# Kernel optimization log

Hardware: AMD Instinct MI355X
Metric: run time of the kernel (lower is better)

Reference implementation:

```python
import jax, jax.numpy as jnp
import numpy as np

B, S = 64, 200
DK = 32           # d_k = d_a = d_e
NQ = 4096         # n_question
NE = 20000        # n_exercise
NAT = 2000
NIT = 2000


def _xavier(k, shape):
    a = float(np.sqrt(6.0 / (shape[0] + shape[1])))
    return jax.random.uniform(k, shape, jnp.float32, -a, a)


def setup_inputs() -> dict:
    key = jax.random.key(0)
    ks = jax.random.split(key, 24)
    d = {}
    d['e_data'] = jax.random.randint(ks[0], (B, S), 0, NE)
    d['at_data'] = jax.random.randint(ks[1], (B, S), 0, NAT)
    d['it_data'] = jax.random.randint(ks[2], (B, S), 0, NIT)
    d['a_data'] = jax.random.randint(ks[3], (B, S), 0, 2).astype(jnp.float32)
    # binary Q-matrix: ~64 skills per exercise on average
    d['q_matrix'] = (jax.random.uniform(ks[4], (NE + 10, NQ + 1)) < (64.0 / NQ)).astype(jnp.float32)
    d['E_e'] = _xavier(ks[5], (NE + 10, DK))
    d['E_at'] = _xavier(ks[6], (NAT + 10, DK))
    d['E_it'] = _xavier(ks[7], (NIT + 10, DK))
    d['W1'] = _xavier(ks[8], (DK, 3 * DK)); d['b1'] = jnp.zeros((DK,), jnp.float32)
    d['W2'] = _xavier(ks[9], (DK, 4 * DK)); d['b2'] = jnp.zeros((DK,), jnp.float32)
    d['W3'] = _xavier(ks[10], (DK, 4 * DK)); d['b3'] = jnp.zeros((DK,), jnp.float32)
    d['W4'] = _xavier(ks[11], (DK, 3 * DK)); d['b4'] = jnp.zeros((DK,), jnp.float32)
    d['W5'] = _xavier(ks[12], (DK, 2 * DK)); d['b5'] = jnp.zeros((DK,), jnp.float32)
    d['h0'] = _xavier(ks[13], (NQ + 1, DK))
    return d


def _forward(e_data, at_data, it_data, a_data, q_matrix, E_e, E_at, E_it,
             W1, b1, W2, b2, W3, b3, W4, b4, W5, b5, h0):
    e_emb = E_e[e_data]                    # [B,S,DK]
    at_emb = E_at[at_data]                 # [B,S,DK]
    it_emb = E_it[it_data]                 # [B,S,DK]
    a_rep = jnp.broadcast_to(a_data[:, :, None], (B, S, DK))  # repeat answer to d_a
    all_learning = jnp.einsum('bsf,kf->bsk', jnp.concatenate([e_emb, at_emb, a_rep], -1), W1) + b1

    h_pre0 = jnp.broadcast_to(h0[None], (B, NQ + 1, DK))
    h_tilde0 = jnp.einsum('bn,bnd->bd', q_matrix[e_data[:, 0]], h_pre0)
    W4h, W4l, W4i = W4[:, :DK], W4[:, DK:2 * DK], W4[:, 2 * DK:]

    def step(carry, xs):
        learning_pre, h_pre, h_tilde_pre = carry
        e_t, it, learning, e_next_emb, e_next = xs
        q_e = q_matrix[e_t]                               # [B,NQ+1] gather
        x = jnp.concatenate([learning_pre, it, learning, h_tilde_pre], -1)  # [B,4DK]
        lg = jnp.tanh(x @ W2.T + b2)
        gl = jax.nn.sigmoid(x @ W3.T + b3)
        LG = gl * (lg + 1.0) * 0.5                        # [B,DK]
        LG_tilde = q_e[:, :, None] * LG[:, None, :]       # scatter (outer product), dropout off (eval)
        gamma_f = jax.nn.sigmoid(h_pre @ W4h.T + (LG @ W4l.T + it @ W4i.T + b4)[:, None, :])
        h = LG_tilde + gamma_f * h_pre                    # [B,NQ+1,DK]
        h_tilde = jnp.einsum('bn,bnd->bd', q_matrix[e_next], h)
        y = jax.nn.sigmoid(jnp.concatenate([e_next_emb, h_tilde], -1) @ W5.T + b5).sum(-1) / DK
        return (learning, h, h_tilde), y

    xs = (e_data[:, :-1].T,
          jnp.swapaxes(it_emb[:, :-1], 0, 1),
          jnp.swapaxes(all_learning[:, :-1], 0, 1),
          jnp.swapaxes(e_emb[:, 1:], 0, 1),
          e_data[:, 1:].T)
    init = (jnp.zeros((B, DK), jnp.float32), h_pre0, h_tilde0)
    _, ys = jax.lax.scan(step, init, xs)                  # ys: [S-1,B]
    pred = jnp.concatenate([jnp.zeros((B, 1), jnp.float32), ys.T], axis=1)
    return pred


def reference(e_data, at_data, it_data, a_data, q_matrix, E_e, E_at, E_it,
              W1, b1, W2, b2, W3, b3, W4, b4, W5, b5, h0):
    return _forward(e_data, at_data, it_data, a_data, q_matrix, E_e, E_at, E_it,
                    W1, b1, W2, b2, W3, b3, W4, b4, W5, b5, h0)
```

## Files before the change

### kernel.cpp

```cpp
#include <hip/hip_runtime.h>

#define Bv    64
#define Sv    200
#define DKv   32
#define NQ1v  4097
#define NWG   8
#define TPB   256
#define ROWS  2
#define NSTEP 199

typedef unsigned long long u64;

__device__ __forceinline__ float fsig(float x) {
  return __builtin_amdgcn_rcpf(1.0f + __builtin_amdgcn_exp2f(x * -1.4426950408889634f));
}
__device__ __forceinline__ float ftanh_(float x) {
  return fmaf(2.0f, fsig(2.0f * x), -1.0f);
}
__device__ __forceinline__ u64 packvt(float v, unsigned tag) {
  return ((u64)tag << 32) | (u64)__float_as_uint(v);
}
__device__ __forceinline__ u64 fresh_read(u64* p) {
  return __hip_atomic_fetch_add(p, 0ull, __ATOMIC_RELAXED, __HIP_MEMORY_SCOPE_AGENT);
}
__device__ __forceinline__ void fresh_write(u64* p, u64 v) {
  (void)__hip_atomic_exchange(p, v, __ATOMIC_RELAXED, __HIP_MEMORY_SCOPE_AGENT);
}

__global__ void lpkt_init(float* out) {
  int i = threadIdx.x;
  if (i < Bv) out[i * Sv] = 0.0f;
}

__global__ __launch_bounds__(TPB, 2) void lpkt_main(
    const int* __restrict__ e_data, const int* __restrict__ at_data,
    const int* __restrict__ it_data, const float* __restrict__ a_data,
    const float* __restrict__ q_matrix,
    const float* __restrict__ E_e, const float* __restrict__ E_at, const float* __restrict__ E_it,
    const float* __restrict__ W1, const float* __restrict__ b1,
    const float* __restrict__ W2, const float* __restrict__ b2,
    const float* __restrict__ W3, const float* __restrict__ b3,
    const float* __restrict__ W4, const float* __restrict__ b4,
    const float* __restrict__ W5, const float* __restrict__ b5,
    const float* __restrict__ h0, float* __restrict__ out,
    u64* __restrict__ partial)
{
  const int tid = threadIdx.x;
  const int wg  = blockIdx.x & (NWG - 1);
  const int b   = blockIdx.x / NWG;
  const int k   = tid & 31;
  const int p   = tid >> 5;
  const int nbase = wg * (TPB * ROWS);

  __shared__ float W23T[128 * 64];
  __shared__ __align__(16) float W1L[32 * 100];
  __shared__ __align__(16) float W4L[32 * 100];
  __shared__ __align__(16) float W5L[32 * 68];
  __shared__ float bL[5 * 32];
  __shared__ __align__(16) float xw_lds[96];
  __shared__ __align__(16) float it_lds[DKv];
  __shared__ __align__(16) float lcA[DKv], lcB[DKv];
  __shared__ __align__(16) float ht_lds[DKv];
  __shared__ __align__(16) float LG_lds[DKv];
  __shared__ __align__(16) float c_lds[DKv];
  __shared__ __align__(16) float red[8][DKv];
  __shared__ __align__(16) float red2[8][DKv];
  __shared__ float ht_part[DKv];
  __shared__ __align__(16) float h49[DKv];

  for (int idx = tid; idx < 128 * 32; idx += TPB) {
    int j = idx & 127, kk = idx >> 7;
    W23T[j * 64 + 2 * kk]     = W2[kk * 128 + j];
    W23T[j * 64 + 2 * kk + 1] = W3[kk * 128 + j];
  }
  for (int idx = tid; idx < 32 * 96; idx += TPB) {
    int r = idx / 96, c = idx % 96;
    W1L[r * 100 + c] = W1[idx];
    W4L[r * 100 + c] = W4[idx];
  }
  for (int idx = tid; idx < 32 * 64; idx += TPB) {
    int r = idx >> 6, c = idx & 63;
    W5L[r * 68 + c] = W5[idx];
  }
  if (tid < 32) {
    bL[0 * 32 + tid] = b1[tid]; bL[1 * 32 + tid] = b2[tid];
    bL[2 * 32 + tid] = b3[tid]; bL[3 * 32 + tid] = b4[tid];
    bL[4 * 32 + tid] = b5[tid];
  }
  if (tid < DKv) { ht_part[tid] = 0.0f; lcB[tid] = 0.0f; }
  if (wg == 0 && tid < DKv) h49[tid] = h0[4096 * DKv + tid];

  float h[ROWS][DKv];
#pragma unroll
  for (int r = 0; r < ROWS; r++) {
    const float4* hp = (const float4*)(h0 + (size_t)(nbase + r * TPB + tid) * DKv);
#pragma unroll
    for (int i = 0; i < 8; i++) {
      float4 v = hp[i];
      h[r][4*i] = v.x; h[r][4*i+1] = v.y; h[r][4*i+2] = v.z; h[r][4*i+3] = v.w;
    }
  }
  const int e0 = e_data[b * Sv];
  const float* q0 = q_matrix + (size_t)e0 * NQ1v;
  float qc[ROWS];
#pragma unroll
  for (int r = 0; r < ROWS; r++) qc[r] = q0[nbase + r * TPB + tid];
  float qc49 = (wg == 0 && tid < DKv) ? q0[4096] : 0.0f;
  __syncthreads();

#pragma unroll
  for (int r = 0; r < ROWS; r++) {
    if (qc[r] != 0.0f) {
#pragma unroll
      for (int kk = 0; kk < DKv; kk++) atomicAdd(&ht_part[kk], h[r][kk]);
    }
  }
  if (wg == 0 && tid < DKv && qc49 != 0.0f) atomicAdd(&ht_part[tid], h49[tid]);
  __syncthreads();
  if (tid < DKv)
    fresh_write(&partial[((size_t)(1 % 3) * Bv + b) * (NWG * DKv) + wg * DKv + tid],
                packvt(ht_part[tid], 1u));

  for (int t = 0; t < NSTEP; t++) {
    float* lc_cur  = (t & 1) ? lcB : lcA;
    float* lc_prev = (t & 1) ? lcA : lcB;
    const unsigned tau_g = (unsigned)(t + 1);
    const unsigned tau_p = (unsigned)(t + 2);

    const int ecur  = e_data[b * Sv + t];
    const int enext = e_data[b * Sv + t + 1];
    const int atc   = at_data[b * Sv + t];
    const int itc   = it_data[b * Sv + t];
    const float av  = a_data[b * Sv + t];
    const float* qnr = q_matrix + (size_t)enext * NQ1v;
    float qn[ROWS];
#pragma unroll
    for (int r = 0; r < ROWS; r++) qn[r] = qnr[nbase + r * TPB + tid];
    float qn49 = (wg == 0 && tid < DKv) ? qnr[4096] : 0.0f;

    if (tid < 96)
      xw_lds[tid] = (tid < 32) ? E_e[(size_t)ecur * DKv + tid]
                  : (tid < 64) ? E_at[(size_t)atc * DKv + (tid - 32)] : av;
    else if (tid < 128)
      it_lds[tid - 96] = E_it[(size_t)itc * DKv + (tid - 96)];

    float acc[ROWS][DKv];
#pragma unroll
    for (int kk = 0; kk < DKv; kk++) {
      float a0 = 0.0f, a1 = 0.0f;
#pragma unroll
      for (int d = 0; d < DKv; d += 4) {
        float4 w = *(const float4*)&W4[kk * 96 + d];
        a0 = fmaf(w.x, h[0][d+0], a0); a1 = fmaf(w.x, h[1][d+0], a1);
        a0 = fmaf(w.y, h[0][d+1], a0); a1 = fmaf(w.y, h[1][d+1], a1);
        a0 = fmaf(w.z, h[0][d+2], a0); a1 = fmaf(w.z, h[1][d+2], a1);
        a0 = fmaf(w.w, h[0][d+3], a0); a1 = fmaf(w.w, h[1][d+3], a1);
      }
      acc[0][kk] = a0; acc[1][kk] = a1;
    }
    __syncthreads();

    if (tid < DKv) {
      u64* pb = partial + ((size_t)(tau_g % 3) * Bv + b) * (NWG * DKv) + tid;
      u64 v[NWG];
      for (;;) {
        bool ok = true;
#pragma unroll
        for (int w2 = 0; w2 < NWG; w2++) {
          v[w2] = fresh_read(&pb[w2 * DKv]);
          ok = ok && ((unsigned)(v[w2] >> 32) == tau_g);
        }
        if (ok) break;
        __builtin_amdgcn_s_sleep(2);
      }
      float s = 0.0f;
#pragma unroll
      for (int w2 = 0; w2 < NWG; w2++) s += __uint_as_float((unsigned)v[w2]);
      ht_lds[tid] = s;
    } else if (tid >= 64 && tid < 96) {
      const int kx = tid - 64;
      float s = bL[0 * 32 + kx];
      const float4* wp = (const float4*)&W1L[kx * 100];
      const float4* xp = (const float4*)xw_lds;
#pragma unroll
      for (int i = 0; i < 24; i++) {
        float4 w = wp[i]; float4 x = xp[i];
        s = fmaf(x.x, w.x, s); s = fmaf(x.y, w.y, s);
        s = fmaf(x.z, w.z, s); s = fmaf(x.w, w.w, s);
      }
      lc_cur[kx] = s;
    }
    __syncthreads();

    {
      const int seg = p >> 1;
      const float* sp = (seg == 0) ? lc_prev : (seg == 1) ? it_lds
                      : (seg == 2) ? lc_cur  : ht_lds;
      const int off = (p & 1) * 16;
      float xv[16];
#pragma unroll
      for (int i = 0; i < 4; i++) {
        float4 v = ((const float4*)(sp + off))[i];
        xv[4*i] = v.x; xv[4*i+1] = v.y; xv[4*i+2] = v.z; xv[4*i+3] = v.w;
      }
      float s2 = 0.0f, s3 = 0.0f;
      const int jb = 16 * p;
#pragma unroll
      for (int i = 0; i < 16; i++) {
        float2 w = *(const float2*)&W23T[(jb + i) * 64 + 2 * k];
        s2 = fmaf(xv[i], w.x, s2);
        s3 = fmaf(xv[i], w.y, s3);
      }
      red[p][k] = s2; red2[p][k] = s3;
    }
    __syncthreads();

    if (tid < DKv) {
      float s2 = bL[1 * 32 + tid], s3 = bL[2 * 32 + tid];
#pragma unroll
      for (int pp = 0; pp < 8; pp++) { s2 += red[pp][tid]; s3 += red2[pp][tid]; }
      LG_lds[tid] = fsig(s3) * (ftanh_(s2) + 1.0f) * 0.5f;
    } else if (tid >= 128 && tid < 160) ht_part[tid - 128] = 0.0f;
    __syncthreads();

    {
      const float* up = (p < 4) ? (LG_lds + 8 * p) : (it_lds + 8 * (p - 4));
      const float4* wp = (const float4*)&W4L[k * 100 + 32 + 8 * p];
      float4 w0 = wp[0], w1 = wp[1];
      float pc = 0.0f;
      pc = fmaf(up[0], w0.x, pc); pc = fmaf(up[1], w0.y, pc);
      pc = fmaf(up[2], w0.z, pc); pc = fmaf(up[3], w0.w, pc);
      pc = fmaf(up[4], w1.x, pc); pc = fmaf(up[5], w1.y, pc);
      pc = fmaf(up[6], w1.z, pc); pc = fmaf(up[7], w1.w, pc);
      red[p][k] = pc;
    }
    if (wg == 0 && t >= 1 && tid >= 64 && tid < 128) {
      const int p2 = p - 2;
      const float* zs = (p2 == 0) ? xw_lds : ht_lds;
      const float4* wp = (const float4*)&W5L[k * 68 + 32 * p2];
      float acc5 = 0.0f;
#pragma unroll
      for (int i = 0; i < 8; i++) {
        float4 w = wp[i]; float4 z = ((const float4*)zs)[i];
        acc5 = fmaf(z.x, w.x, acc5); acc5 = fmaf(z.y, w.y, acc5);
        acc5 = fmaf(z.z, w.z, acc5); acc5 = fmaf(z.w, w.w, acc5);
      }
      red2[p2][k] = acc5;
    }
    __syncthreads();

    if (tid < DKv) {
      float s = bL[3 * 32 + tid];
#pragma unroll
      for (int pp = 0; pp < 8; pp++) s += red[pp][tid];
      c_lds[tid] = s;
    } else if (wg == 0 && t >= 1 && tid >= 96 && tid < 128) {
      const int kx = tid - 96;
      float s = fsig(bL[4 * 32 + kx] + red2[0][kx] + red2[1][kx]);
#pragma unroll
      for (int m = 1; m < 32; m <<= 1) s += __shfl_xor(s, m);
      if (tid == 96) out[b * Sv + t] = s * (1.0f / DKv);
    }
    __syncthreads();

    {
      float c_r[DKv], lg_r[DKv];
#pragma unroll
      for (int i = 0; i < 8; i++) {
        float4 cv = ((const float4*)c_lds)[i];
        float4 gv = ((const float4*)LG_lds)[i];
        c_r[4*i] = cv.x; c_r[4*i+1] = cv.y; c_r[4*i+2] = cv.z; c_r[4*i+3] = cv.w;
        lg_r[4*i] = gv.x; lg_r[4*i+1] = gv.y; lg_r[4*i+2] = gv.z; lg_r[4*i+3] = gv.w;
      }
#pragma unroll
      for (int r = 0; r < ROWS; r++) {
        const float qcr = qc[r];
#pragma unroll
        for (int kk = 0; kk < DKv; kk++) {
          float g = fsig(acc[r][kk] + c_r[kk]);
          h[r][kk] = fmaf(g, h[r][kk], qcr * lg_r[kk]);
        }
        if (qn[r] != 0.0f) {
#pragma unroll
          for (int kk = 0; kk < DKv; kk++) atomicAdd(&ht_part[kk], h[r][kk]);
        }
        qc[r] = qn[r];
      }
    }
    if (wg == 0 && tid < DKv) {
      float hh[DKv];
#pragma unroll
      for (int i = 0; i < 8; i++) {
        float4 v = ((const float4*)h49)[i];
        hh[4*i] = v.x; hh[4*i+1] = v.y; hh[4*i+2] = v.z; hh[4*i+3] = v.w;
      }
      float a = c_lds[tid];
#pragma unroll
      for (int d = 0; d < DKv; d += 4) {
        float4 w = *(const float4*)&W4L[tid * 100 + d];
        a = fmaf(w.x, hh[d+0], a); a = fmaf(w.y, hh[d+1], a);
        a = fmaf(w.z, hh[d+2], a); a = fmaf(w.w, hh[d+3], a);
      }
      float hn = fmaf(fsig(a), h49[tid], qc49 * LG_lds[tid]);
      h49[tid] = hn;
      if (qn49 != 0.0f) atomicAdd(&ht_part[tid], hn);
      qc49 = qn49;
    }
    __syncthreads();

    if (tid < DKv)
      fresh_write(&partial[((size_t)(tau_p % 3) * Bv + b) * (NWG * DKv) + wg * DKv + tid],
                  packvt(ht_part[tid], tau_p));
  }

  if (wg == 0) {
    const unsigned tau_f = (unsigned)(NSTEP + 1);
    if (tid < DKv) {
      u64* pb = partial + ((size_t)(tau_f % 3) * Bv + b) * (NWG * DKv) + tid;
      u64 v[NWG];
      for (;;) {
        bool ok = true;
#pragma unroll
        for (int w2 = 0; w2 < NWG; w2++) {
          v[w2] = fresh_read(&pb[w2 * DKv]);
          ok = ok && ((unsigned)(v[w2] >> 32) == tau_f);
        }
        if (ok) break;
        __builtin_amdgcn_s_sleep(2);
      }
      float s = 0.0f;
#pragma unroll
      for (int w2 = 0; w2 < NWG; w2++) s += __uint_as_float((unsigned)v[w2]);
      ht_lds[tid] = s;
      xw_lds[tid] = E_e[(size_t)e_data[b * Sv + 199] * DKv + tid];
    }
    __syncthreads();
    if (tid >= 64 && tid < 128) {
      const int p2 = p - 2;
      const float* zs = (p2 == 0) ? xw_lds : ht_lds;
      const float4* wp = (const float4*)&W5L[k * 68 + 32 * p2];
      float acc5 = 0.0f;
#pragma unroll
      for (int i = 0; i < 8; i++) {
        float4 w = wp[i]; float4 z = ((const float4*)zs)[i];
        acc5 = fmaf(z.x, w.x, acc5); acc5 = fmaf(z.y, w.y, acc5);
        acc5 = fmaf(z.z, w.z, acc5); acc5 = fmaf(z.w, w.w, acc5);
      }
      red2[p2][k] = acc5;
    }
    __syncthreads();
    if (tid >= 96 && tid < 128) {
      const int kx = tid - 96;
      float s = fsig(bL[4 * 32 + kx] + red2[0][kx] + red2[1][kx]);
#pragma unroll
      for (int m = 1; m < 32; m <<= 1) s += __shfl_xor(s, m);
      if (tid == 96) out[b * Sv + 199] = s * (1.0f / DKv);
    }
  }
}

extern "C" void kernel_launch(void* const* d_in, const int* in_sizes, int n_in,
                              void* d_out, int out_size, void* d_ws, size_t ws_size,
                              hipStream_t stream) {
  const int*   e_data   = (const int*)d_in[0];
  const int*   at_data  = (const int*)d_in[1];
  const int*   it_data  = (const int*)d_in[2];
  const float* a_data   = (const float*)d_in[3];
  const float* q_matrix = (const float*)d_in[4];
  const float* E_e      = (const float*)d_in[5];
  const float* E_at     = (const float*)d_in[6];
  const float* E_it     = (const float*)d_in[7];
  const float* W1 = (const float*)d_in[8];
  const float* b1 = (const float*)d_in[9];
  const float* W2 = (const float*)d_in[10];
  const float* b2 = (const float*)d_in[11];
  const float* W3 = (const float*)d_in[12];
  const float* b3 = (const float*)d_in[13];
  const float* W4 = (const float*)d_in[14];
  const float* b4 = (const float*)d_in[15];
  const float* W5 = (const float*)d_in[16];
  const float* b5 = (const float*)d_in[17];
  const float* h0 = (const float*)d_in[18];
  float* out = (float*)d_out;

  u64* partial = (u64*)d_ws;

  lpkt_init<<<1, 64, 0, stream>>>(out);
  lpkt_main<<<dim3(Bv * NWG), dim3(TPB), 0, stream>>>(
      e_data, at_data, it_data, a_data, q_matrix, E_e, E_at, E_it,
      W1, b1, W2, b2, W3, b3, W4, b4, W5, b5, h0, out, partial);
}
```

Baseline: 4.904 ms.

## Process two batch chains per workgroup to overlap cross-workgroup sync latency

Each workgroup now carries the recurrent state for two batch elements, b and b+32, and runs their per-step chains back to back. The intent is that while one chain waits on the tagged partial-sum exchange with peer workgroups, the other chain's stage makes progress. The grid is halved accordingly. In exchange, the register state per thread doubles (two copies of h) under the same launch bounds, which risks spills or lower occupancy, and each block does twice the serial work per step.

```diff
diff --git a/kernel.cpp b/kernel.cpp
--- a/kernel.cpp
+++ b/kernel.cpp
@@ -10,6 +10,8 @@
 #define NSTEP 199
 
 typedef unsigned long long u64;
+
+template<int I> struct ic { static constexpr int value = I; };
 
 __device__ __forceinline__ float fsig(float x) {
   return __builtin_amdgcn_rcpf(1.0f + __builtin_amdgcn_exp2f(x * -1.4426950408889634f));
@@ -45,11 +47,13 @@
     const float* __restrict__ h0, float* __restrict__ out,
     u64* __restrict__ partial)
 {
-  const int tid = threadIdx.x;
-  const int wg  = blockIdx.x & (NWG - 1);
-  const int b   = blockIdx.x / NWG;
-  const int k   = tid & 31;
-  const int p   = tid >> 5;
+  const int tid  = threadIdx.x;
+  const int wg   = blockIdx.x & (NWG - 1);
+  const int pair = blockIdx.x / NWG;
+  const int bA   = pair;
+  const int bB   = pair + 32;
+  const int k    = tid & 31;
+  const int p    = tid >> 5;
   const int nbase = wg * (TPB * ROWS);
 
   __shared__ float W23T[128 * 64];
@@ -57,16 +61,16 @@
   __shared__ __align__(16) float W4L[32 * 100];
   __shared__ __align__(16) float W5L[32 * 68];
   __shared__ float bL[5 * 32];
-  __shared__ __align__(16) float xw_lds[96];
-  __shared__ __align__(16) float it_lds[DKv];
-  __shared__ __align__(16) float lcA[DKv], lcB[DKv];
-  __shared__ __align__(16) float ht_lds[DKv];
-  __shared__ __align__(16) float LG_lds[DKv];
-  __shared__ __align__(16) float c_lds[DKv];
+  __shared__ __align__(16) float xw_lds[2][96];
+  __shared__ __align__(16) float it_lds[2][DKv];
+  __shared__ __align__(16) float lcA[2][DKv], lcB[2][DKv];
+  __shared__ __align__(16) float ht_lds[2][DKv];
+  __shared__ __align__(16) float LG_lds[2][DKv];
+  __shared__ __align__(16) float c_lds[2][DKv];
   __shared__ __align__(16) float red[8][DKv];
   __shared__ __align__(16) float red2[8][DKv];
-  __shared__ float ht_part[DKv];
-  __shared__ __align__(16) float h49[DKv];
+  __shared__ float ht_part[2][DKv];
+  __shared__ __align__(16) float h49[2][DKv];
 
   for (int idx = tid; idx < 128 * 32; idx += TPB) {
     int j = idx & 127, kk = idx >> 7;
@@ -87,88 +91,285 @@
     bL[2 * 32 + tid] = b3[tid]; bL[3 * 32 + tid] = b4[tid];
     bL[4 * 32 + tid] = b5[tid];
   }
-  if (tid < DKv) { ht_part[tid] = 0.0f; lcB[tid] = 0.0f; }
-  if (wg == 0 && tid < DKv) h49[tid] = h0[4096 * DKv + tid];
-
-  float h[ROWS][DKv];
+  if (tid < DKv) {
+    ht_part[0][tid] = 0.0f; ht_part[1][tid] = 0.0f;
+    lcB[0][tid] = 0.0f;     lcB[1][tid] = 0.0f;
+  }
+  if (wg == 0 && tid < DKv) {
+    float v = h0[4096 * DKv + tid];
+    h49[0][tid] = v; h49[1][tid] = v;
+  }
+
+  float h[2][ROWS][DKv];
 #pragma unroll
   for (int r = 0; r < ROWS; r++) {
     const float4* hp = (const float4*)(h0 + (size_t)(nbase + r * TPB + tid) * DKv);
 #pragma unroll
     for (int i = 0; i < 8; i++) {
       float4 v = hp[i];
-      h[r][4*i] = v.x; h[r][4*i+1] = v.y; h[r][4*i+2] = v.z; h[r][4*i+3] = v.w;
-    }
-  }
-  const int e0 = e_data[b * Sv];
-  const float* q0 = q_matrix + (size_t)e0 * NQ1v;
-  float qc[ROWS];
-#pragma unroll
-  for (int r = 0; r < ROWS; r++) qc[r] = q0[nbase + r * TPB + tid];
-  float qc49 = (wg == 0 && tid < DKv) ? q0[4096] : 0.0f;
+      h[0][r][4*i] = v.x; h[0][r][4*i+1] = v.y; h[0][r][4*i+2] = v.z; h[0][r][4*i+3] = v.w;
+      h[1][r][4*i] = v.x; h[1][r][4*i+1] = v.y; h[1][r][4*i+2] = v.z; h[1][r][4*i+3] = v.w;
+    }
+  }
+  const float* q0A = q_matrix + (size_t)e_data[bA * Sv] * NQ1v;
+  const float* q0B = q_matrix + (size_t)e_data[bB * Sv] * NQ1v;
+  float qc[2][ROWS];
+  float qc49[2] = {0.0f, 0.0f};
+#pragma unroll
+  for (int r = 0; r < ROWS; r++) {
+    qc[0][r] = q0A[nbase + r * TPB + tid];
+    qc[1][r] = q0B[nbase + r * TPB + tid];
+  }
+  if (wg == 0 && tid < DKv) { qc49[0] = q0A[4096]; qc49[1] = q0B[4096]; }
   __syncthreads();
 
 #pragma unroll
-  for (int r = 0; r < ROWS; r++) {
-    if (qc[r] != 0.0f) {
-#pragma unroll
-      for (int kk = 0; kk < DKv; kk++) atomicAdd(&ht_part[kk], h[r][kk]);
-    }
-  }
-  if (wg == 0 && tid < DKv && qc49 != 0.0f) atomicAdd(&ht_part[tid], h49[tid]);
+  for (int bi = 0; bi < 2; bi++) {
+#pragma unroll
+    for (int r = 0; r < ROWS; r++) {
+      if (qc[bi][r] != 0.0f) {
+#pragma unroll
+        for (int kk = 0; kk < DKv; kk++) atomicAdd(&ht_part[bi][kk], h[bi][r][kk]);
+      }
+    }
+    if (wg == 0 && tid < DKv && qc49[bi] != 0.0f) atomicAdd(&ht_part[bi][tid], h49[bi][tid]);
+  }
   __syncthreads();
-  if (tid < DKv)
-    fresh_write(&partial[((size_t)(1 % 3) * Bv + b) * (NWG * DKv) + wg * DKv + tid],
-                packvt(ht_part[tid], 1u));
+  if (tid < DKv) {
+    fresh_write(&partial[((size_t)(1 % 3) * Bv + bA) * (NWG * DKv) + wg * DKv + tid],
+                packvt(ht_part[0][tid], 1u));
+    fresh_write(&partial[((size_t)(1 % 3) * Bv + bB) * (NWG * DKv) + wg * DKv + tid],
+                packvt(ht_part[1][tid], 1u));
+  }
+
+  float acc[ROWS][DKv];
+  float qn[2][ROWS];
+  float qn49[2];
 
   for (int t = 0; t < NSTEP; t++) {
-    float* lc_cur  = (t & 1) ? lcB : lcA;
-    float* lc_prev = (t & 1) ? lcA : lcB;
     const unsigned tau_g = (unsigned)(t + 1);
     const unsigned tau_p = (unsigned)(t + 2);
 
-    const int ecur  = e_data[b * Sv + t];
-    const int enext = e_data[b * Sv + t + 1];
-    const int atc   = at_data[b * Sv + t];
-    const int itc   = it_data[b * Sv + t];
-    const float av  = a_data[b * Sv + t];
-    const float* qnr = q_matrix + (size_t)enext * NQ1v;
-    float qn[ROWS];
-#pragma unroll
-    for (int r = 0; r < ROWS; r++) qn[r] = qnr[nbase + r * TPB + tid];
-    float qn49 = (wg == 0 && tid < DKv) ? qnr[4096] : 0.0f;
-
-    if (tid < 96)
-      xw_lds[tid] = (tid < 32) ? E_e[(size_t)ecur * DKv + tid]
-                  : (tid < 64) ? E_at[(size_t)atc * DKv + (tid - 32)] : av;
-    else if (tid < 128)
-      it_lds[tid - 96] = E_it[(size_t)itc * DKv + (tid - 96)];
-
-    float acc[ROWS][DKv];
-#pragma unroll
-    for (int kk = 0; kk < DKv; kk++) {
-      float a0 = 0.0f, a1 = 0.0f;
-#pragma unroll
-      for (int d = 0; d < DKv; d += 4) {
-        float4 w = *(const float4*)&W4[kk * 96 + d];
-        a0 = fmaf(w.x, h[0][d+0], a0); a1 = fmaf(w.x, h[1][d+0], a1);
-        a0 = fmaf(w.y, h[0][d+1], a0); a1 = fmaf(w.y, h[1][d+1], a1);
-        a0 = fmaf(w.z, h[0][d+2], a0); a1 = fmaf(w.z, h[1][d+2], a1);
-        a0 = fmaf(w.w, h[0][d+3], a0); a1 = fmaf(w.w, h[1][d+3], a1);
-      }
-      acc[0][kk] = a0; acc[1][kk] = a1;
-    }
-    __syncthreads();
-
-    if (tid < DKv) {
-      u64* pb = partial + ((size_t)(tau_g % 3) * Bv + b) * (NWG * DKv) + tid;
+    {
+      const int ecA = e_data[bA * Sv + t], enA = e_data[bA * Sv + t + 1];
+      const int atA = at_data[bA * Sv + t], itA = it_data[bA * Sv + t];
+      const float avA = a_data[bA * Sv + t];
+      const int ecB = e_data[bB * Sv + t], enB = e_data[bB * Sv + t + 1];
+      const int atB = at_data[bB * Sv + t], itB = it_data[bB * Sv + t];
+      const float avB = a_data[bB * Sv + t];
+      const float* qnA = q_matrix + (size_t)enA * NQ1v;
+      const float* qnB = q_matrix + (size_t)enB * NQ1v;
+#pragma unroll
+      for (int r = 0; r < ROWS; r++) {
+        qn[0][r] = qnA[nbase + r * TPB + tid];
+        qn[1][r] = qnB[nbase + r * TPB + tid];
+      }
+      qn49[0] = qn49[1] = 0.0f;
+      if (wg == 0 && tid < DKv) { qn49[0] = qnA[4096]; qn49[1] = qnB[4096]; }
+
+      if (tid < 96)
+        xw_lds[0][tid] = (tid < 32) ? E_e[(size_t)ecA * DKv + tid]
+                       : (tid < 64) ? E_at[(size_t)atA * DKv + (tid - 32)] : avA;
+      else if (tid < 128)
+        it_lds[0][tid - 96] = E_it[(size_t)itA * DKv + (tid - 96)];
+      else if (tid < 224) {
+        int u = tid - 128;
+        xw_lds[1][u] = (u < 32) ? E_e[(size_t)ecB * DKv + u]
+                     : (u < 64) ? E_at[(size_t)atB * DKv + (u - 32)] : avB;
+      } else
+        it_lds[1][tid - 224] = E_it[(size_t)itB * DKv + (tid - 224)];
+    }
+
+    auto chain = [&](auto BIC) {
+      constexpr int BI = decltype(BIC)::value;
+      const int bX = BI ? bB : bA;
+      float* lc_cur  = (t & 1) ? &lcB[BI][0] : &lcA[BI][0];
+      float* lc_prev = (t & 1) ? &lcA[BI][0] : &lcB[BI][0];
+
+#pragma unroll
+      for (int kk = 0; kk < DKv; kk++) {
+        float a0 = 0.0f, a1 = 0.0f;
+#pragma unroll
+        for (int d = 0; d < DKv; d += 4) {
+          float4 w = *(const float4*)&W4[kk * 96 + d];
+          a0 = fmaf(w.x, h[BI][0][d+0], a0); a1 = fmaf(w.x, h[BI][1][d+0], a1);
+          a0 = fmaf(w.y, h[BI][0][d+1], a0); a1 = fmaf(w.y, h[BI][1][d+1], a1);
+          a0 = fmaf(w.z, h[BI][0][d+2], a0); a1 = fmaf(w.z, h[BI][1][d+2], a1);
+          a0 = fmaf(w.w, h[BI][0][d+3], a0); a1 = fmaf(w.w, h[BI][1][d+3], a1);
+        }
+        acc[0][kk] = a0; acc[1][kk] = a1;
+      }
+      __syncthreads();
+
+      if (tid < DKv) {
+        u64* pb = partial + ((size_t)(tau_g % 3) * Bv + bX) * (NWG * DKv) + tid;
+        u64 v[NWG];
+        for (;;) {
+          bool ok = true;
+#pragma unroll
+          for (int w2 = 0; w2 < NWG; w2++) {
+            v[w2] = fresh_read(&pb[w2 * DKv]);
+            ok = ok && ((unsigned)(v[w2] >> 32) == tau_g);
+          }
+          if (ok) break;
+          __builtin_amdgcn_s_sleep(2);
+        }
+        float s = 0.0f;
+#pragma unroll
+        for (int w2 = 0; w2 < NWG; w2++) s += __uint_as_float((unsigned)v[w2]);
+        ht_lds[BI][tid] = s;
+      } else if (tid >= 64 && tid < 96) {
+        const int kx = tid - 64;
+        float s = bL[0 * 32 + kx];
+        const float4* wp = (const float4*)&W1L[kx * 100];
+        const float4* xp = (const float4*)&xw_lds[BI][0];
+#pragma unroll
+        for (int i = 0; i < 24; i++) {
+          float4 w = wp[i]; float4 x = xp[i];
+          s = fmaf(x.x, w.x, s); s = fmaf(x.y, w.y, s);
+          s = fmaf(x.z, w.z, s); s = fmaf(x.w, w.w, s);
+        }
+        lc_cur[kx] = s;
+      }
+      __syncthreads();
+
+      {
+        const int seg = p >> 1;
+        const float* sp = (seg == 0) ? lc_prev : (seg == 1) ? &it_lds[BI][0]
+                        : (seg == 2) ? lc_cur  : &ht_lds[BI][0];
+        const int off = (p & 1) * 16;
+        float xv[16];
+#pragma unroll
+        for (int i = 0; i < 4; i++) {
+          float4 v = ((const float4*)(sp + off))[i];
+          xv[4*i] = v.x; xv[4*i+1] = v.y; xv[4*i+2] = v.z; xv[4*i+3] = v.w;
+        }
+        float s2 = 0.0f, s3 = 0.0f;
+        const int jb = 16 * p;
+#pragma unroll
+        for (int i = 0; i < 16; i++) {
+          float2 w = *(const float2*)&W23T[(jb + i) * 64 + 2 * k];
+          s2 = fmaf(xv[i], w.x, s2);
+          s3 = fmaf(xv[i], w.y, s3);
+        }
+        red[p][k] = s2; red2[p][k] = s3;
+      }
+      __syncthreads();
+
+      if (tid < DKv) {
+        float s2 = bL[1 * 32 + tid], s3 = bL[2 * 32 + tid];
+#pragma unroll
+        for (int pp = 0; pp < 8; pp++) { s2 += red[pp][tid]; s3 += red2[pp][tid]; }
+        LG_lds[BI][tid] = fsig(s3) * (ftanh_(s2) + 1.0f) * 0.5f;
+      } else if (tid >= 128 && tid < 160) ht_part[BI][tid - 128] = 0.0f;
+      __syncthreads();
+
+      {
+        const float* up = (p < 4) ? &LG_lds[BI][8 * p] : &it_lds[BI][8 * (p - 4)];
+        const float4* wp = (const float4*)&W4L[k * 100 + 32 + 8 * p];
+        float4 w0 = wp[0], w1 = wp[1];
+        float pc = 0.0f;
+        pc = fmaf(up[0], w0.x, pc); pc = fmaf(up[1], w0.y, pc);
+        pc = fmaf(up[2], w0.z, pc); pc = fmaf(up[3], w0.w, pc);
+        pc = fmaf(up[4], w1.x, pc); pc = fmaf(up[5], w1.y, pc);
+        pc = fmaf(up[6], w1.z, pc); pc = fmaf(up[7], w1.w, pc);
+        red[p][k] = pc;
+      }
+      if (wg == 0 && t >= 1 && tid >= 64 && tid < 128) {
+        const int p2 = p - 2;
+        const float* zs = (p2 == 0) ? &xw_lds[BI][0] : &ht_lds[BI][0];
+        const float4* wp = (const float4*)&W5L[k * 68 + 32 * p2];
+        float acc5 = 0.0f;
+#pragma unroll
+        for (int i = 0; i < 8; i++) {
+          float4 w = wp[i]; float4 z = ((const float4*)zs)[i];
+          acc5 = fmaf(z.x, w.x, acc5); acc5 = fmaf(z.y, w.y, acc5);
+          acc5 = fmaf(z.z, w.z, acc5); acc5 = fmaf(z.w, w.w, acc5);
+        }
+        red2[p2][k] = acc5;
+      }
+      __syncthreads();
+
+      if (tid < DKv) {
+        float s = bL[3 * 32 + tid];
+#pragma unroll
+        for (int pp = 0; pp < 8; pp++) s += red[pp][tid];
+        c_lds[BI][tid] = s;
+      } else if (wg == 0 && t >= 1 && tid >= 96 && tid < 128) {
+        const int kx = tid - 96;
+        float s = fsig(bL[4 * 32 + kx] + red2[0][kx] + red2[1][kx]);
+#pragma unroll
+        for (int m = 1; m < 32; m <<= 1) s += __shfl_xor(s, m);
+        if (tid == 96) out[bX * Sv + t] = s * (1.0f / DKv);
+      }
+      __syncthreads();
+
+#pragma unroll
+      for (int r = 0; r < ROWS; r++) {
+        const float qcr = qc[BI][r];
+#pragma unroll
+        for (int kq = 0; kq < 8; kq++) {
+          float4 cv = ((const float4*)&c_lds[BI][0])[kq];
+          float4 gv = ((const float4*)&LG_lds[BI][0])[kq];
+          float g0 = fsig(acc[r][4*kq+0] + cv.x);
+          float g1 = fsig(acc[r][4*kq+1] + cv.y);
+          float g2 = fsig(acc[r][4*kq+2] + cv.z);
+          float g3 = fsig(acc[r][4*kq+3] + cv.w);
+          h[BI][r][4*kq+0] = fmaf(g0, h[BI][r][4*kq+0], qcr * gv.x);
+          h[BI][r][4*kq+1] = fmaf(g1, h[BI][r][4*kq+1], qcr * gv.y);
+          h[BI][r][4*kq+2] = fmaf(g2, h[BI][r][4*kq+2], qcr * gv.z);
+          h[BI][r][4*kq+3] = fmaf(g3, h[BI][r][4*kq+3], qcr * gv.w);
+        }
+        if (qn[BI][r] != 0.0f) {
+#pragma unroll
+          for (int kk = 0; kk < DKv; kk++) atomicAdd(&ht_part[BI][kk], h[BI][r][kk]);
+        }
+        qc[BI][r] = qn[BI][r];
+      }
+      if (wg == 0 && tid < DKv) {
+        float hh[DKv];
+#pragma unroll
+        for (int i = 0; i < 8; i++) {
+          float4 v = ((const float4*)&h49[BI][0])[i];
+          hh[4*i] = v.x; hh[4*i+1] = v.y; hh[4*i+2] = v.z; hh[4*i+3] = v.w;
+        }
+        float a = c_lds[BI][tid];
+#pragma unroll
+        for (int d = 0; d < DKv; d += 4) {
+          float4 w = *(const float4*)&W4L[tid * 100 + d];
+          a = fmaf(w.x, hh[d+0], a); a = fmaf(w.y, hh[d+1], a);
+          a = fmaf(w.z, hh[d+2], a); a = fmaf(w.w, hh[d+3], a);
+        }
+        float hn = fmaf(fsig(a), h49[BI][tid], qc49[BI] * LG_lds[BI][tid]);
+        h49[BI][tid] = hn;
+        if (qn49[BI] != 0.0f) atomicAdd(&ht_part[BI][tid], hn);
+        qc49[BI] = qn49[BI];
+      }
+      __syncthreads();
+
+      if (tid < DKv)
+        fresh_write(&partial[((size_t)(tau_p % 3) * Bv + bX) * (NWG * DKv) + wg * DKv + tid],
+                    packvt(ht_part[BI][tid], tau_p));
+    };
+
+    chain(ic<0>{});
+    chain(ic<1>{});
+  }
+
+  if (wg == 0) {
+    const unsigned tau_f = (unsigned)(NSTEP + 1);
+    const int bi = (tid >= 128) ? 1 : 0;
+    const int lane = tid & 127;
+    const int bX = bi ? bB : bA;
+    if (lane < DKv) {
+      u64* pb = partial + ((size_t)(tau_f % 3) * Bv + bX) * (NWG * DKv) + lane;
       u64 v[NWG];
       for (;;) {
         bool ok = true;
 #pragma unroll
         for (int w2 = 0; w2 < NWG; w2++) {
           v[w2] = fresh_read(&pb[w2 * DKv]);
-          ok = ok && ((unsigned)(v[w2] >> 32) == tau_g);
+          ok = ok && ((unsigned)(v[w2] >> 32) == tau_f);
         }
         if (ok) break;
         __builtin_amdgcn_s_sleep(2);
@@ -176,185 +377,32 @@
       float s = 0.0f;
 #pragma unroll
       for (int w2 = 0; w2 < NWG; w2++) s += __uint_as_float((unsigned)v[w2]);
-      ht_lds[tid] = s;
-    } else if (tid >= 64 && tid < 96) {
-      const int kx = tid - 64;
-      float s = bL[0 * 32 + kx];
-      const float4* wp = (const float4*)&W1L[kx * 100];
-      const float4* xp = (const float4*)xw_lds;
-#pragma unroll
-      for (int i = 0; i < 24; i++) {
-        float4 w = wp[i]; float4 x = xp[i];
-        s = fmaf(x.x, w.x, s); s = fmaf(x.y, w.y, s);
-        s = fmaf(x.z, w.z, s); s = fmaf(x.w, w.w, s);
-      }
-      lc_cur[kx] = s;
+      ht_lds[bi][lane] = s;
+      xw_lds[bi][lane] = E_e[(size_t)e_data[bX * Sv + 199] * DKv + lane];
     }
     __syncthreads();
-
-    {
-      const int seg = p >> 1;
-      const float* sp = (seg == 0) ? lc_prev : (seg == 1) ? it_lds
-                      : (seg == 2) ? lc_cur  : ht_lds;
-      const int off = (p & 1) * 16;
-      float xv[16];
-#pragma unroll
-      for (int i = 0; i < 4; i++) {
-        float4 v = ((const float4*)(sp + off))[i];
-        xv[4*i] = v.x; xv[4*i+1] = v.y; xv[4*i+2] = v.z; xv[4*i+3] = v.w;
-      }
-      float s2 = 0.0f, s3 = 0.0f;
-      const int jb = 16 * p;
-#pragma unroll
-      for (int i = 0; i < 16; i++) {
-        float2 w = *(const float2*)&W23T[(jb + i) * 64 + 2 * k];
-        s2 = fmaf(xv[i], w.x, s2);
-        s3 = fmaf(xv[i], w.y, s3);
-      }
-      red[p][k] = s2; red2[p][k] = s3;
+    if (lane >= 64) {
+      const int p2 = ((lane >> 5) & 3) - 2;
+      if (p2 >= 0 && lane < 128) {
+        const float* zs = (p2 == 0) ? &xw_lds[bi][0] : &ht_lds[bi][0];
+        const float4* wp = (const float4*)&W5L[k * 68 + 32 * p2];
+        float acc5 = 0.0f;
+#pragma unroll
+        for (int i = 0; i < 8; i++) {
+          float4 w = wp[i]; float4 z = ((const float4*)zs)[i];
+          acc5 = fmaf(z.x, w.x, acc5); acc5 = fmaf(z.y, w.y, acc5);
+          acc5 = fmaf(z.z, w.z, acc5); acc5 = fmaf(z.w, w.w, acc5);
+        }
+        red2[bi * 2 + p2][k] = acc5;
+      }
     }
     __syncthreads();
-
-    if (tid < DKv) {
-      float s2 = bL[1 * 32 + tid], s3 = bL[2 * 32 + tid];
-#pragma unroll
-      for (int pp = 0; pp < 8; pp++) { s2 += red[pp][tid]; s3 += red2[pp][tid]; }
-      LG_lds[tid] = fsig(s3) * (ftanh_(s2) + 1.0f) * 0.5f;
-    } else if (tid >= 128 && tid < 160) ht_part[tid - 128] = 0.0f;
-    __syncthreads();
-
-    {
-      const float* up = (p < 4) ? (LG_lds + 8 * p) : (it_lds + 8 * (p - 4));
-      const float4* wp = (const float4*)&W4L[k * 100 + 32 + 8 * p];
-      float4 w0 = wp[0], w1 = wp[1];
-      float pc = 0.0f;
-      pc = fmaf(up[0], w0.x, pc); pc = fmaf(up[1], w0.y, pc);
-      pc = fmaf(up[2], w0.z, pc); pc = fmaf(up[3], w0.w, pc);
-      pc = fmaf(up[4], w1.x, pc); pc = fmaf(up[5], w1.y, pc);
-      pc = fmaf(up[6], w1.z, pc); pc = fmaf(up[7], w1.w, pc);
-      red[p][k] = pc;
-    }
-    if (wg == 0 && t >= 1 && tid >= 64 && tid < 128) {
-      const int p2 = p - 2;
-      const float* zs = (p2 == 0) ? xw_lds : ht_lds;
-      const float4* wp = (const float4*)&W5L[k * 68 + 32 * p2];
-      float acc5 = 0.0f;
-#pragma unroll
-      for (int i = 0; i < 8; i++) {
-        float4 w = wp[i]; float4 z = ((const float4*)zs)[i];
-        acc5 = fmaf(z.x, w.x, acc5); acc5 = fmaf(z.y, w.y, acc5);
-        acc5 = fmaf(z.z, w.z, acc5); acc5 = fmaf(z.w, w.w, acc5);
-      }
-      red2[p2][k] = acc5;
-    }
-    __syncthreads();
-
-    if (tid < DKv) {
-      float s = bL[3 * 32 + tid];
-#pragma unroll
-      for (int pp = 0; pp < 8; pp++) s += red[pp][tid];
-      c_lds[tid] = s;
-    } else if (wg == 0 && t >= 1 && tid >= 96 && tid < 128) {
-      const int kx = tid - 96;
-      float s = fsig(bL[4 * 32 + kx] + red2[0][kx] + red2[1][kx]);
+    if (lane >= 96 && lane < 128) {
+      const int kx = lane - 96;
+      float s = fsig(bL[4 * 32 + kx] + red2[bi * 2 + 0][kx] + red2[bi * 2 + 1][kx]);
 #pragma unroll
       for (int m = 1; m < 32; m <<= 1) s += __shfl_xor(s, m);
-      if (tid == 96) out[b * Sv + t] = s * (1.0f / DKv);
-    }
-    __syncthreads();
-
-    {
-      float c_r[DKv], lg_r[DKv];
-#pragma unroll
-      for (int i = 0; i < 8; i++) {
-        float4 cv = ((const float4*)c_lds)[i];
-        float4 gv = ((const float4*)LG_lds)[i];
-        c_r[4*i] = cv.x; c_r[4*i+1] = cv.y; c_r[4*i+2] = cv.z; c_r[4*i+3] = cv.w;
-        lg_r[4*i] = gv.x; lg_r[4*i+1] = gv.y; lg_r[4*i+2] = gv.z; lg_r[4*i+3] = gv.w;
-      }
-#pragma unroll
-      for (int r = 0; r < ROWS; r++) {
-        const float qcr = qc[r];
-#pragma unroll
-        for (int kk = 0; kk < DKv; kk++) {
-          float g = fsig(acc[r][kk] + c_r[kk]);
-          h[r][kk] = fmaf(g, h[r][kk], qcr * lg_r[kk]);
-        }
-        if (qn[r] != 0.0f) {
-#pragma unroll
-          for (int kk = 0; kk < DKv; kk++) atomicAdd(&ht_part[kk], h[r][kk]);
-        }
-        qc[r] = qn[r];
-      }
-    }
-    if (wg == 0 && tid < DKv) {
-      float hh[DKv];
-#pragma unroll
-      for (int i = 0; i < 8; i++) {
-        float4 v = ((const float4*)h49)[i];
-        hh[4*i] = v.x; hh[4*i+1] = v.y; hh[4*i+2] = v.z; hh[4*i+3] = v.w;
-      }
-      float a = c_lds[tid];
-#pragma unroll
-      for (int d = 0; d < DKv; d += 4) {
-        float4 w = *(const float4*)&W4L[tid * 100 + d];
-        a = fmaf(w.x, hh[d+0], a); a = fmaf(w.y, hh[d+1], a);
-        a = fmaf(w.z, hh[d+2], a); a = fmaf(w.w, hh[d+3], a);
-      }
-      float hn = fmaf(fsig(a), h49[tid], qc49 * LG_lds[tid]);
-      h49[tid] = hn;
-      if (qn49 != 0.0f) atomicAdd(&ht_part[tid], hn);
-      qc49 = qn49;
-    }
-    __syncthreads();
-
-    if (tid < DKv)
-      fresh_write(&partial[((size_t)(tau_p % 3) * Bv + b) * (NWG * DKv) + wg * DKv + tid],
-                  packvt(ht_part[tid], tau_p));
-  }
-
-  if (wg == 0) {
-    const unsigned tau_f = (unsigned)(NSTEP + 1);
-    if (tid < DKv) {
-      u64* pb = partial + ((size_t)(tau_f % 3) * Bv + b) * (NWG * DKv) + tid;
-      u64 v[NWG];
-      for (;;) {
-        bool ok = true;
-#pragma unroll
-        for (int w2 = 0; w2 < NWG; w2++) {
-          v[w2] = fresh_read(&pb[w2 * DKv]);
-          ok = ok && ((unsigned)(v[w2] >> 32) == tau_f);
-        }
-        if (ok) break;
-        __builtin_amdgcn_s_sleep(2);
-      }
-      float s = 0.0f;
-#pragma unroll
-      for (int w2 = 0; w2 < NWG; w2++) s += __uint_as_float((unsigned)v[w2]);
-      ht_lds[tid] = s;
-      xw_lds[tid] = E_e[(size_t)e_data[b * Sv + 199] * DKv + tid];
-    }
-    __syncthreads();
-    if (tid >= 64 && tid < 128) {
-      const int p2 = p - 2;
-      const float* zs = (p2 == 0) ? xw_lds : ht_lds;
-      const float4* wp = (const float4*)&W5L[k * 68 + 32 * p2];
-      float acc5 = 0.0f;
-#pragma unroll
-      for (int i = 0; i < 8; i++) {
-        float4 w = wp[i]; float4 z = ((const float4*)zs)[i];
-        acc5 = fmaf(z.x, w.x, acc5); acc5 = fmaf(z.y, w.y, acc5);
-        acc5 = fmaf(z.z, w.z, acc5); acc5 = fmaf(z.w, w.w, acc5);
-      }
-      red2[p2][k] = acc5;
-    }
-    __syncthreads();
-    if (tid >= 96 && tid < 128) {
-      const int kx = tid - 96;
-      float s = fsig(bL[4 * 32 + kx] + red2[0][kx] + red2[1][kx]);
-#pragma unroll
-      for (int m = 1; m < 32; m <<= 1) s += __shfl_xor(s, m);
-      if (tid == 96) out[b * Sv + 199] = s * (1.0f / DKv);
+      if (kx == 0) out[bX * Sv + 199] = s * (1.0f / DKv);
     }
   }
 }
@@ -386,7 +434,7 @@
   u64* partial = (u64*)d_ws;
 
   lpkt_init<<<1, 64, 0, stream>>>(out);
-  lpkt_main<<<dim3(Bv * NWG), dim3(TPB), 0, stream>>>(
+  lpkt_main<<<dim3((Bv / 2) * NWG), dim3(TPB), 0, stream>>>(
       e_data, at_data, it_data, a_data, q_matrix, E_e, E_at, E_it,
       W1, b1, W2, b2, W3, b3, W4, b4, W5, b5, h0, out, partial);
 }
```

After: 8.109 ms. 1.65x slower.
